# Optimization experiments

Measured on AMD Instinct MI355X. Metric: run time of the kernel, lower is better.

The kernel has to match this reference:

```python
import jax, jax.numpy as jnp
import numpy as np

N = 10000        # nodes
E = 320000       # edges (before self-loops)
F_IN = 128       # num_feature
H1, C1 = 16, 16  # GAT1: heads=16, out=16 -> concat 256
D = 256          # GAT2: heads=1, out=256
G = 64           # graphs in batch
L = 10           # num_label
NEG_SLOPE = 0.2


def setup_inputs() -> dict:
    key = jax.random.key(0)
    ks = jax.random.split(key, 13)
    sc = lambda f: 1.0 / np.sqrt(f)
    inp = {
        "x": jax.random.normal(ks[0], (N, F_IN), jnp.float32),
        "edge_index": jax.random.randint(ks[1], (2, E), 0, N, dtype=jnp.int32),
        "batch": jnp.sort(jax.random.randint(ks[2], (N,), 0, G, dtype=jnp.int32)),
        "W1": jax.random.normal(ks[3], (F_IN, H1 * C1), jnp.float32) * sc(F_IN),
        "a_src1": jax.random.normal(ks[4], (H1, C1), jnp.float32) * sc(C1),
        "a_dst1": jax.random.normal(ks[5], (H1, C1), jnp.float32) * sc(C1),
        "b1": jnp.zeros((H1 * C1,), jnp.float32),
        "W2": jax.random.normal(ks[6], (H1 * C1, D), jnp.float32) * sc(H1 * C1),
        "a_src2": jax.random.normal(ks[7], (1, D), jnp.float32) * sc(D),
        "a_dst2": jax.random.normal(ks[8], (1, D), jnp.float32) * sc(D),
        "b2": jnp.zeros((D,), jnp.float32),
        "lin_w": jax.random.normal(ks[9], (D, L), jnp.float32) * sc(D),
        "lin_b": jnp.zeros((L,), jnp.float32),
    }
    return inp


def _leaky(v):
    return jnp.where(v >= 0, v, NEG_SLOPE * v)


def gat_conv(x, src, dst, W, a_src, a_dst, bias, heads, ch):
    """PyG GATConv (eval mode): gather, leaky-relu logits, segment softmax over dst, scatter-add."""
    n = x.shape[0]
    h = (x @ W).reshape(n, heads, ch)                       # [N,H,C]
    al_s = jnp.sum(h * a_src, axis=-1)                      # [N,H]
    al_d = jnp.sum(h * a_dst, axis=-1)                      # [N,H]
    e = _leaky(al_s[src] + al_d[dst])                       # [Etot,H]
    m = jax.ops.segment_max(e, dst, num_segments=n)         # [N,H]
    m = jnp.where(jnp.isfinite(m), m, 0.0)
    ex = jnp.exp(e - m[dst])
    s = jax.ops.segment_sum(ex, dst, num_segments=n)        # [N,H] (>0: self-loops)
    alpha = ex / s[dst]                                     # [Etot,H]
    out = jax.ops.segment_sum(alpha[:, :, None] * h[src], dst, num_segments=n)
    return out.reshape(n, heads * ch) + bias


def reference(x, edge_index, batch, W1, a_src1, a_dst1, b1, W2, a_src2, a_dst2, b2, lin_w, lin_b):
    n = x.shape[0]
    loops = jnp.arange(n, dtype=edge_index.dtype)
    src = jnp.concatenate([edge_index[0], loops])           # add_self_loops=True (PyG default)
    dst = jnp.concatenate([edge_index[1], loops])

    h = gat_conv(x, src, dst, W1, a_src1, a_dst1, b1, H1, C1)
    h = jax.nn.relu(h)
    h = gat_conv(h, src, dst, W2, a_src2, a_dst2, b2, 1, D)

    # global_mean_pool over graph ids
    sums = jax.ops.segment_sum(h, batch, num_segments=G)    # [G,D]
    cnts = jax.ops.segment_sum(jnp.ones((n,), h.dtype), batch, num_segments=G)
    pooled = sums / jnp.maximum(cnts, 1.0)[:, None]

    # dropout is identity in eval mode
    return pooled @ lin_w + lin_b                           # [G,L]
```

## Files before the change

### kernel.cpp

```cpp
#include <hip/hip_runtime.h>
#include <hip/hip_bf16.h>
#include <math.h>

#define NEG_SLOPE 0.2f
#define LDS_FENCE() asm volatile("s_waitcnt lgkmcnt(0)" ::: "memory")

#define CSR_NB 128
#define CSR_CAP 2048
#define XC_NB 128
#define W1T_NB 32
#define WT_NB 64

__device__ __forceinline__ ushort f2bf(float f) {
    uint x = __float_as_uint(f);
    x += 0x7fffu + ((x >> 16) & 1u);
    return (ushort)(x >> 16);
}
__device__ __forceinline__ float bf2f(ushort u) {
    return __uint_as_float((uint)u << 16);
}

typedef __attribute__((ext_vector_type(8))) short bf16x8v;
typedef __attribute__((ext_vector_type(4))) float f32x4;

__global__ __launch_bounds__(256) void k_prep(
    const int* __restrict__ ei, int E, int N, int NP, int CE,
    int* __restrict__ gcount, int* __restrict__ tmp,
    const float* __restrict__ x, ushort* __restrict__ Xb,
    const float* __restrict__ W1, ushort* __restrict__ W1t,
    const float* __restrict__ W2, ushort* __restrict__ Wt) {
    __shared__ float smem[32 * 33];
    int t = threadIdx.x;
    if (blockIdx.x < CSR_NB) {
        int* lhist = (int*)smem;
        int b = blockIdx.x;
        for (int p = t; p < 384; p += 256) lhist[p] = 0;
        __syncthreads();
        int Etot = E + N;
        int e0 = b * CE, e1 = min(Etot, e0 + CE);
        for (int e = e0 + t; e < e1; e += 256) {
            int d = (e < E) ? ei[E + e] : (e - E);
            atomicAdd(&lhist[d >> 5], 1);
        }
        __syncthreads();
        for (int p = t; p < NP; p += 256) {
            int c = lhist[p];
            lhist[p] = c ? atomicAdd(&gcount[p], c) : 0;
        }
        __syncthreads();
        for (int e = e0 + t; e < e1; e += 256) {
            int s, d;
            if (e < E) { s = ei[e]; d = ei[E + e]; } else { s = d = e - E; }
            int p = d >> 5;
            int pos = atomicAdd(&lhist[p], 1);
            tmp[p * CSR_CAP + min(pos, CSR_CAP - 1)] = (s << 5) | (d & 31);
        }
    } else if (blockIdx.x < CSR_NB + XC_NB) {
        int b = blockIdx.x - CSR_NB;
        int nfl4 = N * 32;
        int stride = XC_NB * 256;
        for (int i = b * 256 + t; i < nfl4; i += stride) {
            float4 v = ((const float4*)x)[i];
            ushort4 u;
            u.x = f2bf(v.x); u.y = f2bf(v.y); u.z = f2bf(v.z); u.w = f2bf(v.w);
            ((ushort4*)Xb)[i] = u;
        }
    } else if (blockIdx.x < CSR_NB + XC_NB + W1T_NB) {
        float (*tile)[33] = (float (*)[33])smem;
        int tb = blockIdx.x - CSR_NB - XC_NB;
        int k0 = (tb >> 3) * 32, j0 = (tb & 7) * 32;
        int c = t & 31, i0 = t >> 5;
#pragma unroll
        for (int p = 0; p < 4; ++p) {
            int i = i0 + p * 8;
            tile[i][c] = W1[(size_t)(k0 + i) * 256 + j0 + c];
        }
        __syncthreads();
#pragma unroll
        for (int p = 0; p < 4; ++p) {
            int i = i0 + p * 8;
            W1t[(size_t)(j0 + i) * 128 + k0 + c] = f2bf(tile[c][i]);
        }
    } else {
        float (*tile)[33] = (float (*)[33])smem;
        int tb = blockIdx.x - CSR_NB - XC_NB - W1T_NB;
        int k0 = (tb >> 3) * 32, j0 = (tb & 7) * 32;
        int c = t & 31, i0 = t >> 5;
#pragma unroll
        for (int p = 0; p < 4; ++p) {
            int i = i0 + p * 8;
            tile[i][c] = W2[(size_t)(k0 + i) * 256 + j0 + c];
        }
        __syncthreads();
#pragma unroll
        for (int p = 0; p < 4; ++p) {
            int i = i0 + p * 8;
            Wt[(size_t)(j0 + i) * 256 + k0 + c] = f2bf(tile[c][i]);
        }
    }
}

__device__ __forceinline__ void gemm1_mfma_body(int bx,
    const ushort* __restrict__ Xb, const ushort* __restrict__ W1t,
    ushort* __restrict__ Cb, const float* __restrict__ as1,
    const float* __restrict__ ad1, float* __restrict__ als,
    float* __restrict__ ald, int N) {
    int t = threadIdx.x, lane = t & 63, w = t >> 6;
    int n0 = bx * 16;
    int l15 = lane & 15, kb = lane >> 4;
    int col0 = w * 64;
    int arow = min(n0 + l15, N - 1);
    const ushort* Xp = Xb + (size_t)arow * 128 + kb * 8;
    f32x4 acc[4] = {f32x4{0,0,0,0}, f32x4{0,0,0,0}, f32x4{0,0,0,0}, f32x4{0,0,0,0}};
#pragma unroll
    for (int ks = 0; ks < 4; ++ks) {
        bf16x8v a = *(const bf16x8v*)(Xp + ks * 32);
#pragma unroll
        for (int tt = 0; tt < 4; ++tt) {
            const ushort* Bp = W1t + (size_t)(col0 + tt * 16 + l15) * 128 + ks * 32 + kb * 8;
            bf16x8v b = *(const bf16x8v*)Bp;
            acc[tt] = __builtin_amdgcn_mfma_f32_16x16x32_bf16(a, b, acc[tt], 0, 0, 0);
        }
    }
#pragma unroll
    for (int r = 0; r < 4; ++r) {
        int n = n0 + kb * 4 + r;
#pragma unroll
        for (int tt = 0; tt < 4; ++tt) {
            int col = col0 + tt * 16 + l15;
            float v = acc[tt][r];
            float s = v * as1[col];
            float d = v * ad1[col];
            s += __shfl_xor(s, 1); s += __shfl_xor(s, 2);
            s += __shfl_xor(s, 4); s += __shfl_xor(s, 8);
            d += __shfl_xor(d, 1); d += __shfl_xor(d, 2);
            d += __shfl_xor(d, 4); d += __shfl_xor(d, 8);
            if (n < N) {
                Cb[(size_t)n * 256 + col] = f2bf(v);
                if (l15 == 0) {
                    als[n * 16 + (col >> 4)] = s;
                    ald[n * 16 + (col >> 4)] = d;
                }
            }
        }
    }
}

__global__ __launch_bounds__(256) void k_g1f(
    const int* __restrict__ tmp, const int* __restrict__ gcount,
    int2* __restrict__ rowse, int* __restrict__ col, int NP,
    const ushort* __restrict__ Xb, const ushort* __restrict__ W1t,
    ushort* __restrict__ Cb, const float* __restrict__ as1,
    const float* __restrict__ ad1, float* __restrict__ als1,
    float* __restrict__ ald1, int N) {
    if ((int)blockIdx.x >= NP) {
        gemm1_mfma_body(blockIdx.x - NP, Xb, W1t, Cb, as1, ad1, als1, ald1, N);
        return;
    }
    __shared__ int dcnt[32], dcur[32];
    int t = threadIdx.x, p = blockIdx.x;
    int base = p * CSR_CAP;
    int cnt = min(gcount[p], CSR_CAP);
    if (t < 32) dcnt[t] = 0;
    __syncthreads();
    for (int i = t; i < cnt; i += 256) atomicAdd(&dcnt[tmp[base + i] & 31], 1);
    __syncthreads();
    if (t < 32) {
        int v = dcnt[t];
        int x = v;
#pragma unroll
        for (int off = 1; off < 32; off <<= 1) {
            int u = __shfl_up(x, off);
            if (t >= off) x += u;
        }
        int excl = x - v;
        dcur[t] = excl;
        int dst = (p << 5) + t;
        if (dst < N) rowse[dst] = make_int2(base + excl, base + excl + v);
    }
    __syncthreads();
    for (int i = t; i < cnt; i += 256) {
        int v = tmp[base + i];
        int pos = atomicAdd(&dcur[v & 31], 1);
        col[base + pos] = v >> 5;
    }
}

__global__ __launch_bounds__(256) void k_gemm2_mfma(
    const ushort* __restrict__ Xb, const ushort* __restrict__ Wt,
    ushort* __restrict__ Cb, const float* __restrict__ as2,
    const float* __restrict__ ad2, float* __restrict__ als,
    float* __restrict__ ald, int N) {
    __shared__ float red[4][16][2];
    int t = threadIdx.x, lane = t & 63, w = t >> 6;
    int n0 = blockIdx.x * 16;
    int l15 = lane & 15, kb = lane >> 4;
    int col0 = w * 64;
    int arow = min(n0 + l15, N - 1);
    const ushort* Xp = Xb + (size_t)arow * 256 + kb * 8;
    f32x4 acc[4] = {f32x4{0,0,0,0}, f32x4{0,0,0,0}, f32x4{0,0,0,0}, f32x4{0,0,0,0}};
#pragma unroll
    for (int ks = 0; ks < 8; ++ks) {
        bf16x8v a = *(const bf16x8v*)(Xp + ks * 32);
#pragma unroll
        for (int tt = 0; tt < 4; ++tt) {
            const ushort* Bp = Wt + (size_t)(col0 + tt * 16 + l15) * 256 + ks * 32 + kb * 8;
            bf16x8v b = *(const bf16x8v*)Bp;
            acc[tt] = __builtin_amdgcn_mfma_f32_16x16x32_bf16(a, b, acc[tt], 0, 0, 0);
        }
    }
#pragma unroll
    for (int r = 0; r < 4; ++r) {
        int n = n0 + kb * 4 + r;
        float s = 0.f, d = 0.f;
#pragma unroll
        for (int tt = 0; tt < 4; ++tt) {
            int col = col0 + tt * 16 + l15;
            float v = acc[tt][r];
            if (n < N) Cb[(size_t)n * 256 + col] = f2bf(v);
            s += v * as2[col];
            d += v * ad2[col];
        }
        s += __shfl_xor(s, 1); s += __shfl_xor(s, 2);
        s += __shfl_xor(s, 4); s += __shfl_xor(s, 8);
        d += __shfl_xor(d, 1); d += __shfl_xor(d, 2);
        d += __shfl_xor(d, 4); d += __shfl_xor(d, 8);
        if (l15 == 0) { red[w][kb * 4 + r][0] = s; red[w][kb * 4 + r][1] = d; }
    }
    __syncthreads();
    if (t < 16) {
        int n = n0 + t;
        if (n < N) {
            als[n] = red[0][t][0] + red[1][t][0] + red[2][t][0] + red[3][t][0];
            ald[n] = red[0][t][1] + red[1][t][1] + red[2][t][1] + red[3][t][1];
        }
    }
}

__global__ __launch_bounds__(256) void k_gather_h1(
    const int2* __restrict__ rowse, const int* __restrict__ col,
    const ushort* __restrict__ Hb, const float* __restrict__ als,
    const float* __restrict__ ald, const float* __restrict__ bias,
    ushort* __restrict__ outb, int N) {
    int wave = threadIdx.x >> 6, lane = threadIdx.x & 63;
    int n = blockIdx.x * 4 + wave;
    if (n >= N) return;
    int2 se2 = rowse[n];
    int start = se2.x, end = se2.y;
    float aldv = ald[n];
    float4 acc = {0.f, 0.f, 0.f, 0.f};
    float swsum = 0.f;
    const ushort* Hl = Hb + lane * 4;
    for (int base = start; base < end; base += 64) {
        int len = min(64, end - base);
        int s_r = 0;
        float w_r = 0.f;
        if (lane < len) {
            s_r = col[base + lane];
            float v = als[s_r] + aldv;
            v = v >= 0.f ? v : NEG_SLOPE * v;
            w_r = __expf(v);
        }
        swsum += w_r;
        int len8 = (len + 7) & ~7;
        for (int e = 0; e < len8; e += 8) {
            const ushort* hp[8];
            float we[8];
#pragma unroll
            for (int j = 0; j < 8; ++j) {
                hp[j] = Hl + (size_t)__shfl(s_r, e + j) * 256;
                we[j] = __shfl(w_r, e + j);
            }
            ushort4 uv[8];
#pragma unroll
            for (int j = 0; j < 8; ++j) uv[j] = *(const ushort4*)hp[j];
#pragma unroll
            for (int j = 0; j < 8; ++j) {
                acc.x = fmaf(we[j], bf2f(uv[j].x), acc.x);
                acc.y = fmaf(we[j], bf2f(uv[j].y), acc.y);
                acc.z = fmaf(we[j], bf2f(uv[j].z), acc.z);
                acc.w = fmaf(we[j], bf2f(uv[j].w), acc.w);
            }
        }
    }
#pragma unroll
    for (int off = 32; off >= 1; off >>= 1) swsum += __shfl_xor(swsum, off);
    float inv = 1.0f / swsum;
    float4 bv = *(const float4*)(bias + lane * 4);
    ushort4 o;
    o.x = f2bf(fmaf(acc.x, inv, bv.x));
    o.y = f2bf(fmaf(acc.y, inv, bv.y));
    o.z = f2bf(fmaf(acc.z, inv, bv.z));
    o.w = f2bf(fmaf(acc.w, inv, bv.w));
    *(ushort4*)(outb + (size_t)n * 256 + lane * 4) = o;
}

__global__ __launch_bounds__(256) void k_gather_h16(
    const int2* __restrict__ rowse, const int* __restrict__ col,
    const ushort* __restrict__ Hb, const float* __restrict__ als,
    const float* __restrict__ ald, const float* __restrict__ bias,
    ushort* __restrict__ outb, int N) {
    __shared__ float w_lds[4][64 * 16];
    int wave = threadIdx.x >> 6, lane = threadIdx.x & 63;
    int n = blockIdx.x * 4 + wave;
    if (n >= N) return;
    int2 se2 = rowse[n];
    int start = se2.x, end = se2.y;
    int hq = lane & 15;
    int eq = lane >> 4;
    float aldW = ald[n * 16 + hq];
    float4 acc = {0.f, 0.f, 0.f, 0.f};
    float swp = 0.f;
    const ushort* Hl = Hb + lane * 4;
    for (int base = start; base < end; base += 64) {
        int len = min(64, end - base);
        int s_r = (lane < len) ? col[base + lane] : 0;
#pragma unroll
        for (int k = 0; k < 16; ++k) {
            int esub = (k << 2) + eq;
            int s = __shfl(s_r, esub);
            float w = 0.f;
            if (esub < len) {
                float v = als[s * 16 + hq] + aldW;
                v = v >= 0.f ? v : NEG_SLOPE * v;
                w = __expf(v);
            }
            w_lds[wave][(esub << 4) + hq] = w;
            swp += w;
        }
        LDS_FENCE();
        int len8 = (len + 7) & ~7;
        for (int e = 0; e < len8; e += 8) {
            const ushort* hp[8];
            float we[8];
#pragma unroll
            for (int j = 0; j < 8; ++j) {
                hp[j] = Hl + (size_t)__shfl(s_r, e + j) * 256;
                we[j] = w_lds[wave][((e + j) << 4) + (lane >> 2)];
            }
            ushort4 uv[8];
#pragma unroll
            for (int j = 0; j < 8; ++j) uv[j] = *(const ushort4*)hp[j];
#pragma unroll
            for (int j = 0; j < 8; ++j) {
                acc.x = fmaf(we[j], bf2f(uv[j].x), acc.x);
                acc.y = fmaf(we[j], bf2f(uv[j].y), acc.y);
                acc.z = fmaf(we[j], bf2f(uv[j].z), acc.z);
                acc.w = fmaf(we[j], bf2f(uv[j].w), acc.w);
            }
        }
        LDS_FENCE();
    }
    swp += __shfl_xor(swp, 16);
    swp += __shfl_xor(swp, 32);
    float inv = 1.0f / __shfl(swp, lane >> 2);
    float4 bv = *(const float4*)(bias + lane * 4);
    ushort4 o;
    o.x = f2bf(fmaxf(fmaf(acc.x, inv, bv.x), 0.f));
    o.y = f2bf(fmaxf(fmaf(acc.y, inv, bv.y), 0.f));
    o.z = f2bf(fmaxf(fmaf(acc.z, inv, bv.z), 0.f));
    o.w = f2bf(fmaxf(fmaf(acc.w, inv, bv.w), 0.f));
    *(ushort4*)(outb + (size_t)n * 256 + lane * 4) = o;
}

__device__ __forceinline__ int lower_bound_i(const int* __restrict__ a, int n, int v) {
    int lo = 0, hi = n;
    while (lo < hi) {
        int mid = (lo + hi) >> 1;
        if (a[mid] < v) lo = mid + 1; else hi = mid;
    }
    return lo;
}

__global__ __launch_bounds__(1024) void k_pool_final(const ushort* __restrict__ Bb,
                                                     const int* __restrict__ batch,
                                                     const float* __restrict__ lw,
                                                     const float* __restrict__ lb,
                                                     float* __restrict__ out,
                                                     int N, int L) {
    __shared__ float psum[4][256];
    __shared__ float csum[256];
    int t = threadIdx.x;
    int c = t & 255, q = t >> 8;
    int g = blockIdx.x;
    int lo = lower_bound_i(batch, N, g);
    int hi = lower_bound_i(batch, N, g + 1);
    int len = hi - lo;
    int per = (len + 3) >> 2;
    int s0 = lo + q * per, s1 = min(hi, s0 + per);
    float acc = 0.f;
    for (int r = s0; r < s1; ++r) acc += bf2f(Bb[(size_t)r * 256 + c]);
    psum[q][c] = acc;
    __syncthreads();
    if (t < 256) csum[t] = psum[0][t] + psum[1][t] + psum[2][t] + psum[3][t];
    __syncthreads();
    int wave = t >> 6, lane = t & 63;
    if (wave < L) {
        int l = wave;
        float a = csum[lane] * lw[lane * L + l] +
                  csum[lane + 64] * lw[(lane + 64) * L + l] +
                  csum[lane + 128] * lw[(lane + 128) * L + l] +
                  csum[lane + 192] * lw[(lane + 192) * L + l];
#pragma unroll
        for (int off = 32; off >= 1; off >>= 1) a += __shfl_xor(a, off);
        if (lane == 0) out[g * L + l] = a / fmaxf((float)len, 1.0f) + lb[l];
    }
}

extern "C" void kernel_launch(void* const* d_in, const int* in_sizes, int n_in,
                              void* d_out, int out_size, void* d_ws, size_t ws_size,
                              hipStream_t stream) {
    const float* x   = (const float*)d_in[0];
    const int*   ei  = (const int*)d_in[1];
    const int*   bat = (const int*)d_in[2];
    const float* W1  = (const float*)d_in[3];
    const float* as1 = (const float*)d_in[4];
    const float* ad1 = (const float*)d_in[5];
    const float* b1  = (const float*)d_in[6];
    const float* W2  = (const float*)d_in[7];
    const float* as2 = (const float*)d_in[8];
    const float* ad2 = (const float*)d_in[9];
    const float* b2  = (const float*)d_in[10];
    const float* lw  = (const float*)d_in[11];
    const float* lb  = (const float*)d_in[12];
    float* out = (float*)d_out;

    const int N = in_sizes[2];
    const int E = in_sizes[1] / 2;
    const int G = 64, L = 10;
    const int Etot = E + N;
    const int NP = (N + 31) >> 5;
    const int CE = (Etot + CSR_NB - 1) / CSR_NB;

    float* A    = (float*)d_ws;
    float* B    = A + (size_t)N * 256;
    float* als1 = B + (size_t)N * 256;
    float* ald1 = als1 + (size_t)N * 16;
    float* als2 = ald1 + (size_t)N * 16;
    float* ald2 = als2 + N;
    int2* rowse = (int2*)(ald2 + N);
    int* col    = (int*)(rowse + N);
    int* tmp    = col + (size_t)NP * CSR_CAP;
    int* gcount = tmp + (size_t)NP * CSR_CAP;
    ushort* Wt  = (ushort*)(((uintptr_t)(gcount + NP) + 63) & ~(uintptr_t)63);
    ushort* W1t = Wt + 256 * 256;
    ushort* Xb  = W1t + 256 * 128;
    ushort* Abf = (ushort*)A;
    ushort* Bbf = (ushort*)B;

    const int BS = 256;
    auto nb = [](int n, int b) { return (n + b - 1) / b; };
    int nodes4 = nb(N, 4);
    int rows16 = nb(N, 16);

    hipMemsetAsync(gcount, 0, NP * sizeof(int), stream);
    k_prep<<<CSR_NB + XC_NB + W1T_NB + WT_NB, BS, 0, stream>>>(
        ei, E, N, NP, CE, gcount, tmp, x, Xb, W1, W1t, W2, Wt);

    k_g1f<<<NP + rows16, BS, 0, stream>>>(tmp, gcount, rowse, col, NP,
                                          Xb, W1t, Abf, as1, ad1, als1, ald1, N);

    k_gather_h16<<<nodes4, BS, 0, stream>>>(rowse, col, Abf, als1, ald1, b1, Bbf, N);

    k_gemm2_mfma<<<rows16, BS, 0, stream>>>(Bbf, Wt, Abf, as2, ad2, als2, ald2, N);
    k_gather_h1<<<nodes4, BS, 0, stream>>>(rowse, col, Abf, als2, ald2, b2, Bbf, N);

    k_pool_final<<<G, 1024, 0, stream>>>(Bbf, bat, lw, lb, out, N, L);
}
```

Measured before the change: 195.2 us.

## Fuse fp32-to-bf16 conversion into GEMM1 and co-schedule it with CSR scatter

Removes the separate x and W1 bf16 conversion/transpose passes. GEMM1 now reads fp32 x and W1 directly and converts them to bf16 in registers. GEMM1 blocks move into the first kernel, running alongside the edge scatter and W2 transpose, and CSR finalisation becomes its own kernel. The intent is to cut an intermediate buffer round-trip and overlap the GEMM with the scatter. The cost is strided, uncoalesced 4-byte W1 loads (8 per MFMA operand), repeated in every block.

Measured after the change: 193.0 us. Within noise of the previous version (-1.1%).

```diff
diff --git a/kernel.cpp b/kernel.cpp
--- a/kernel.cpp
+++ b/kernel.cpp
@@ -7,8 +7,6 @@
 
 #define CSR_NB 128
 #define CSR_CAP 2048
-#define XC_NB 128
-#define W1T_NB 32
 #define WT_NB 64
 
 __device__ __forceinline__ ushort f2bf(float f) {
@@ -23,85 +21,8 @@
 typedef __attribute__((ext_vector_type(8))) short bf16x8v;
 typedef __attribute__((ext_vector_type(4))) float f32x4;
 
-__global__ __launch_bounds__(256) void k_prep(
-    const int* __restrict__ ei, int E, int N, int NP, int CE,
-    int* __restrict__ gcount, int* __restrict__ tmp,
-    const float* __restrict__ x, ushort* __restrict__ Xb,
-    const float* __restrict__ W1, ushort* __restrict__ W1t,
-    const float* __restrict__ W2, ushort* __restrict__ Wt) {
-    __shared__ float smem[32 * 33];
-    int t = threadIdx.x;
-    if (blockIdx.x < CSR_NB) {
-        int* lhist = (int*)smem;
-        int b = blockIdx.x;
-        for (int p = t; p < 384; p += 256) lhist[p] = 0;
-        __syncthreads();
-        int Etot = E + N;
-        int e0 = b * CE, e1 = min(Etot, e0 + CE);
-        for (int e = e0 + t; e < e1; e += 256) {
-            int d = (e < E) ? ei[E + e] : (e - E);
-            atomicAdd(&lhist[d >> 5], 1);
-        }
-        __syncthreads();
-        for (int p = t; p < NP; p += 256) {
-            int c = lhist[p];
-            lhist[p] = c ? atomicAdd(&gcount[p], c) : 0;
-        }
-        __syncthreads();
-        for (int e = e0 + t; e < e1; e += 256) {
-            int s, d;
-            if (e < E) { s = ei[e]; d = ei[E + e]; } else { s = d = e - E; }
-            int p = d >> 5;
-            int pos = atomicAdd(&lhist[p], 1);
-            tmp[p * CSR_CAP + min(pos, CSR_CAP - 1)] = (s << 5) | (d & 31);
-        }
-    } else if (blockIdx.x < CSR_NB + XC_NB) {
-        int b = blockIdx.x - CSR_NB;
-        int nfl4 = N * 32;
-        int stride = XC_NB * 256;
-        for (int i = b * 256 + t; i < nfl4; i += stride) {
-            float4 v = ((const float4*)x)[i];
-            ushort4 u;
-            u.x = f2bf(v.x); u.y = f2bf(v.y); u.z = f2bf(v.z); u.w = f2bf(v.w);
-            ((ushort4*)Xb)[i] = u;
-        }
-    } else if (blockIdx.x < CSR_NB + XC_NB + W1T_NB) {
-        float (*tile)[33] = (float (*)[33])smem;
-        int tb = blockIdx.x - CSR_NB - XC_NB;
-        int k0 = (tb >> 3) * 32, j0 = (tb & 7) * 32;
-        int c = t & 31, i0 = t >> 5;
-#pragma unroll
-        for (int p = 0; p < 4; ++p) {
-            int i = i0 + p * 8;
-            tile[i][c] = W1[(size_t)(k0 + i) * 256 + j0 + c];
-        }
-        __syncthreads();
-#pragma unroll
-        for (int p = 0; p < 4; ++p) {
-            int i = i0 + p * 8;
-            W1t[(size_t)(j0 + i) * 128 + k0 + c] = f2bf(tile[c][i]);
-        }
-    } else {
-        float (*tile)[33] = (float (*)[33])smem;
-        int tb = blockIdx.x - CSR_NB - XC_NB - W1T_NB;
-        int k0 = (tb >> 3) * 32, j0 = (tb & 7) * 32;
-        int c = t & 31, i0 = t >> 5;
-#pragma unroll
-        for (int p = 0; p < 4; ++p) {
-            int i = i0 + p * 8;
-            tile[i][c] = W2[(size_t)(k0 + i) * 256 + j0 + c];
-        }
-        __syncthreads();
-#pragma unroll
-        for (int p = 0; p < 4; ++p) {
-            int i = i0 + p * 8;
-            Wt[(size_t)(j0 + i) * 256 + k0 + c] = f2bf(tile[c][i]);
-        }
-    }
-}
-
 __device__ __forceinline__ void gemm1_mfma_body(int bx,
-    const ushort* __restrict__ Xb, const ushort* __restrict__ W1t,
+    const float* __restrict__ x, const float* __restrict__ W1,
     ushort* __restrict__ Cb, const float* __restrict__ as1,
     const float* __restrict__ ad1, float* __restrict__ als,
     float* __restrict__ ald, int N) {
@@ -110,15 +31,24 @@
     int l15 = lane & 15, kb = lane >> 4;
     int col0 = w * 64;
     int arow = min(n0 + l15, N - 1);
-    const ushort* Xp = Xb + (size_t)arow * 128 + kb * 8;
+    const float* Xp = x + (size_t)arow * 128 + kb * 8;
     f32x4 acc[4] = {f32x4{0,0,0,0}, f32x4{0,0,0,0}, f32x4{0,0,0,0}, f32x4{0,0,0,0}};
 #pragma unroll
     for (int ks = 0; ks < 4; ++ks) {
-        bf16x8v a = *(const bf16x8v*)(Xp + ks * 32);
+        float4 xa = *(const float4*)(Xp + ks * 32);
+        float4 xc = *(const float4*)(Xp + ks * 32 + 4);
+        bf16x8v a;
+        a[0] = (short)f2bf(xa.x); a[1] = (short)f2bf(xa.y);
+        a[2] = (short)f2bf(xa.z); a[3] = (short)f2bf(xa.w);
+        a[4] = (short)f2bf(xc.x); a[5] = (short)f2bf(xc.y);
+        a[6] = (short)f2bf(xc.z); a[7] = (short)f2bf(xc.w);
 #pragma unroll
         for (int tt = 0; tt < 4; ++tt) {
-            const ushort* Bp = W1t + (size_t)(col0 + tt * 16 + l15) * 128 + ks * 32 + kb * 8;
-            bf16x8v b = *(const bf16x8v*)Bp;
+            int col = col0 + tt * 16 + l15;
+            const float* Wp = W1 + (size_t)(ks * 32 + kb * 8) * 256 + col;
+            bf16x8v b;
+#pragma unroll
+            for (int j = 0; j < 8; ++j) b[j] = (short)f2bf(Wp[(size_t)j * 256]);
             acc[tt] = __builtin_amdgcn_mfma_f32_16x16x32_bf16(a, b, acc[tt], 0, 0, 0);
         }
     }
@@ -146,17 +76,64 @@
     }
 }
 
-__global__ __launch_bounds__(256) void k_g1f(
-    const int* __restrict__ tmp, const int* __restrict__ gcount,
-    int2* __restrict__ rowse, int* __restrict__ col, int NP,
-    const ushort* __restrict__ Xb, const ushort* __restrict__ W1t,
-    ushort* __restrict__ Cb, const float* __restrict__ as1,
-    const float* __restrict__ ad1, float* __restrict__ als1,
-    float* __restrict__ ald1, int N) {
-    if ((int)blockIdx.x >= NP) {
-        gemm1_mfma_body(blockIdx.x - NP, Xb, W1t, Cb, as1, ad1, als1, ald1, N);
-        return;
-    }
+__global__ __launch_bounds__(256) void k_scatter_gemm1(
+    const int* __restrict__ ei, int E, int N, int NP, int CE,
+    int* __restrict__ gcount, int* __restrict__ tmp,
+    const float* __restrict__ x, const float* __restrict__ W1, ushort* __restrict__ A,
+    const float* __restrict__ as1, const float* __restrict__ ad1,
+    float* __restrict__ als1, float* __restrict__ ald1,
+    const float* __restrict__ W2, ushort* __restrict__ Wt) {
+    __shared__ float smem[32 * 33];
+    int t = threadIdx.x;
+    if (blockIdx.x < CSR_NB) {
+        int* lhist = (int*)smem;
+        int b = blockIdx.x;
+        for (int p = t; p < 384; p += 256) lhist[p] = 0;
+        __syncthreads();
+        int Etot = E + N;
+        int e0 = b * CE, e1 = min(Etot, e0 + CE);
+        for (int e = e0 + t; e < e1; e += 256) {
+            int d = (e < E) ? ei[E + e] : (e - E);
+            atomicAdd(&lhist[d >> 5], 1);
+        }
+        __syncthreads();
+        for (int p = t; p < NP; p += 256) {
+            int c = lhist[p];
+            lhist[p] = c ? atomicAdd(&gcount[p], c) : 0;
+        }
+        __syncthreads();
+        for (int e = e0 + t; e < e1; e += 256) {
+            int s, d;
+            if (e < E) { s = ei[e]; d = ei[E + e]; } else { s = d = e - E; }
+            int p = d >> 5;
+            int pos = atomicAdd(&lhist[p], 1);
+            tmp[p * CSR_CAP + min(pos, CSR_CAP - 1)] = (s << 5) | (d & 31);
+        }
+    } else if (blockIdx.x < CSR_NB + WT_NB) {
+        float (*tile)[33] = (float (*)[33])smem;
+        int tb = blockIdx.x - CSR_NB;
+        int k0 = (tb >> 3) * 32, j0 = (tb & 7) * 32;
+        int c = t & 31, i0 = t >> 5;
+#pragma unroll
+        for (int p = 0; p < 4; ++p) {
+            int i = i0 + p * 8;
+            tile[i][c] = W2[(size_t)(k0 + i) * 256 + j0 + c];
+        }
+        __syncthreads();
+#pragma unroll
+        for (int p = 0; p < 4; ++p) {
+            int i = i0 + p * 8;
+            Wt[(size_t)(j0 + i) * 256 + k0 + c] = f2bf(tile[c][i]);
+        }
+    } else {
+        gemm1_mfma_body(blockIdx.x - CSR_NB - WT_NB, x, W1, A, as1, ad1, als1, ald1, N);
+    }
+}
+
+__global__ __launch_bounds__(256) void k_csr_final(const int* __restrict__ tmp,
+                                                   const int* __restrict__ gcount,
+                                                   int2* __restrict__ rowse,
+                                                   int* __restrict__ col, int N) {
     __shared__ int dcnt[32], dcur[32];
     int t = threadIdx.x, p = blockIdx.x;
     int base = p * CSR_CAP;
@@ -443,8 +420,6 @@
     int* tmp    = col + (size_t)NP * CSR_CAP;
     int* gcount = tmp + (size_t)NP * CSR_CAP;
     ushort* Wt  = (ushort*)(((uintptr_t)(gcount + NP) + 63) & ~(uintptr_t)63);
-    ushort* W1t = Wt + 256 * 256;
-    ushort* Xb  = W1t + 256 * 128;
     ushort* Abf = (ushort*)A;
     ushort* Bbf = (ushort*)B;
 
@@ -454,11 +429,9 @@
     int rows16 = nb(N, 16);
 
     hipMemsetAsync(gcount, 0, NP * sizeof(int), stream);
-    k_prep<<<CSR_NB + XC_NB + W1T_NB + WT_NB, BS, 0, stream>>>(
-        ei, E, N, NP, CE, gcount, tmp, x, Xb, W1, W1t, W2, Wt);
-
-    k_g1f<<<NP + rows16, BS, 0, stream>>>(tmp, gcount, rowse, col, NP,
-                                          Xb, W1t, Abf, as1, ad1, als1, ald1, N);
+    k_scatter_gemm1<<<CSR_NB + WT_NB + rows16, BS, 0, stream>>>(
+        ei, E, N, NP, CE, gcount, tmp, x, W1, Abf, as1, ad1, als1, ald1, W2, Wt);
+    k_csr_final<<<NP, BS, 0, stream>>>(tmp, gcount, rowse, col, N);
 
     k_gather_h16<<<nodes4, BS, 0, stream>>>(rowse, col, Abf, als1, ald1, b1, Bbf, N);
 
```
